# Kernel optimization log

Measured on AMD Instinct MI355X. Metric: run time of the kernel, lower is better.

## Reference

```python
import jax, jax.numpy as jnp
import numpy as np

B, L, E, H = 4, 2048, 1024, 16
D = E // H  # head_dim = 64
NEG_INF = -1e9


def _rope(x):
    # x: [B, L, H, D]; standard rotate-half RoPE over head_dim
    seq = x.shape[1]
    inv_freq = 1.0 / (10000.0 ** (jnp.arange(0, D, 2, dtype=jnp.float32) / D))  # [D/2]
    ang = jnp.arange(seq, dtype=jnp.float32)[:, None] * inv_freq               # [L, D/2]
    cos = jnp.concatenate([jnp.cos(ang), jnp.cos(ang)], axis=-1)[None, :, None, :]
    sin = jnp.concatenate([jnp.sin(ang), jnp.sin(ang)], axis=-1)[None, :, None, :]
    x1, x2 = jnp.split(x, 2, axis=-1)
    rot = jnp.concatenate([-x2, x1], axis=-1)
    return x * cos + rot * sin


def setup_inputs() -> dict:
    key = jax.random.key(0)
    ks = jax.random.split(key, 12)
    xavier = lambda k: jax.random.uniform(k, (E, E), jnp.float32,
                                          -np.sqrt(6.0 / (E + E)), np.sqrt(6.0 / (E + E)))
    return {
        "query": jax.random.normal(ks[0], (B, L, E), jnp.float32),
        "key": jax.random.normal(ks[1], (B, L, E), jnp.float32),
        "value": jax.random.normal(ks[2], (B, L, E), jnp.float32),
        "wq": xavier(ks[3]), "bq": jnp.zeros((E,), jnp.float32),
        "wk": xavier(ks[4]), "bk": jnp.zeros((E,), jnp.float32),
        "wv": xavier(ks[5]), "bv": jnp.zeros((E,), jnp.float32),
        "wo": xavier(ks[6]), "bo": jnp.zeros((E,), jnp.float32),
        "key_padding_mask": jax.random.randint(ks[7], (B, L), 0, 2).astype(bool),
    }


def reference(query, key, value, wq, bq, wk, bk, wv, bv, wo, bo, key_padding_mask):
    b, ql = query.shape[0], query.shape[1]
    sl = key.shape[1]
    q = (query @ wq.T + bq).reshape(b, ql, H, D)
    k = (key @ wk.T + bk).reshape(b, sl, H, D)
    v = (value @ wv.T + bv).reshape(b, sl, H, D)
    q = _rope(q)
    k = _rope(k)
    # causal mask (is_causal=True, attn_mask=None path) + key padding mask, additive
    causal = jnp.where(jnp.triu(jnp.ones((ql, sl), bool), k=1), NEG_INF, 0.0)  # [L, L]
    kpm = jnp.where(key_padding_mask[:, None, None, :], NEG_INF, 0.0)          # [B,1,1,S]
    mask = causal[None, None, :, :] + kpm
    scores = jnp.einsum("bqhd,bkhd->bhqk", q, k) / np.sqrt(D) + mask
    attn = jax.nn.softmax(scores, axis=-1)
    out = jnp.einsum("bhqk,bkhd->bqhd", attn, v).reshape(b, ql, E)
    return out @ wo.T + bo
```

## Files before the change

### kernel.cpp

```cpp
#include <hip/hip_runtime.h>

typedef unsigned short u16;
typedef unsigned int   u32;

using bf16x8 = __attribute__((ext_vector_type(8))) __bf16;
using f32x4  = __attribute__((ext_vector_type(4))) float;
using f32x16 = __attribute__((ext_vector_type(16))) float;

#define DEV static __device__ __forceinline__
#define GP(p) (const __attribute__((address_space(1))) void*)(p)
#define LP(p) (__attribute__((address_space(3))) void*)(p)
#define WAITB(N) asm volatile("s_waitcnt vmcnt(" N ")\n\ts_barrier" ::: "memory")

DEV u16 f2bf(float f){
  u32 u = __builtin_bit_cast(u32, f);
  u32 r = u + 0x7fffu + ((u>>16)&1u);
  return (u16)(r>>16);
}
DEV bf16x8 as_bf(uint4 v){ return __builtin_bit_cast(bf16x8, v); }
DEV u32 cvt_pk(float lo, float hi){
  u32 r;
  asm("v_cvt_pk_bf16_f32 %0, %1, %2" : "=v"(r) : "v"(lo), "v"(hi));
  return r;
}
DEV void plswap(u32 &a, u32 &b){
  auto r = __builtin_amdgcn_permlane32_swap((int)a, (int)b, false, false);
  a = (u32)r[0]; b = (u32)r[1];
}
DEV float fexp2(float x){ float r; asm("v_exp_f32 %0, %1" : "=v"(r) : "v"(x)); return r; }
DEV float max3f(float a, float b, float c){
  float r; asm("v_max3_f32 %0, %1, %2, %3" : "=v"(r) : "v"(a), "v"(b), "v"(c)); return r;
}

constexpr int CB = 4, CL = 2048, CE = 1024, CH = 16, CD = 64;
constexpr int CM = CB*CL;
constexpr float LOG2E  = 1.44269504088896f;
constexpr float NEGBIG = -1.44269504e9f;

__global__ void detect_mask_kernel(const void* __restrict__ mask, int* __restrict__ flag){
  __shared__ int a_gt1, a_badf, a_oddnz, a_evennz;
  if (threadIdx.x==0){ a_gt1=0; a_badf=0; a_oddnz=0; a_evennz=0; }
  __syncthreads();
  const u32* w = (const u32*)mask;
  int gt1=0, badf=0, oddnz=0, evennz=0;
  for (int i=threadIdx.x; i<2048; i+=256){
    u32 v = w[i];
    if (v > 1u) gt1 = 1;
    if (v != 0u && v != 0x3f800000u) badf = 1;
    if (v != 0u){ if (i & 1) oddnz = 1; else evennz = 1; }
  }
  if (gt1) atomicOr(&a_gt1,1);
  if (badf) atomicOr(&a_badf,1);
  if (oddnz) atomicOr(&a_oddnz,1);
  if (evennz) atomicOr(&a_evennz,1);
  __syncthreads();
  if (threadIdx.x==0){
    int mode;
    if (!a_gt1)           mode = (!a_oddnz && a_evennz) ? 3 : 0;
    else if (!a_badf)     mode = 1;
    else                  mode = 2;
    flag[0] = mode;
  }
}

__global__ void convert_mask_kernel(const void* __restrict__ mask, const int* __restrict__ flag,
                                    float* __restrict__ maskf){
  int i = blockIdx.x*blockDim.x + threadIdx.x;
  if (i >= CB*CL) return;
  int mode = flag[0];
  int v;
  if      (mode==0) v = ((const int*)mask)[i] != 0;
  else if (mode==1) v = ((const float*)mask)[i] != 0.f;
  else if (mode==3) v = ((const int*)mask)[2*i] != 0;
  else              v = ((const unsigned char*)mask)[i] != 0;
  maskf[i] = v ? NEGBIG : 0.f;
}

__global__ void cast_all(const float* __restrict__ q, const float* __restrict__ k,
                         const float* __restrict__ v,
                         const float* __restrict__ wq, const float* __restrict__ wk,
                         const float* __restrict__ wv, const float* __restrict__ wo,
                         u16* __restrict__ oq, u16* __restrict__ ok, u16* __restrict__ ov,
                         u16* __restrict__ owq, u16* __restrict__ owk,
                         u16* __restrict__ owv, u16* __restrict__ owo){
  int i = blockIdx.x*blockDim.x + threadIdx.x;
  const float* in; u16* out; int j;
  if (i < 3*(1<<21)){
    int w = i >> 21; j = i & ((1<<21)-1);
    in = (w==0)?q:(w==1)?k:v; out = (w==0)?oq:(w==1)?ok:ov;
  } else {
    int r = i - 3*(1<<21);
    int w = r >> 18; j = r & ((1<<18)-1);
    in = (w==0)?wq:(w==1)?wk:(w==2)?wv:wo; out = (w==0)?owq:(w==1)?owk:(w==2)?owv:owo;
  }
  float4 a = ((const float4*)in)[j];
  ushort4 h;
  h.x = f2bf(a.x); h.y = f2bf(a.y); h.z = f2bf(a.z); h.w = f2bf(a.w);
  ((ushort4*)out)[j] = h;
}

__global__ __launch_bounds__(256) void gemm_qkv(
    const u16* __restrict__ qbf, const u16* __restrict__ kbf, const u16* __restrict__ vbf,
    const u16* __restrict__ wqb, const u16* __restrict__ wkb, const u16* __restrict__ wvb,
    const float* __restrict__ bq, const float* __restrict__ bk, const float* __restrict__ bv,
    u16* __restrict__ Qp, u16* __restrict__ Kp, u16* __restrict__ Vt, int zbase)
{
  __shared__ u16 As[2][8192];
  __shared__ u16 Bs[2][8192];
  const int z = zbase + blockIdx.y;
  const int tid=threadIdx.x, lane=tid&63, wid=tid>>6;
  const int llo=lane&15, lhi=lane>>4;
  const u16* A; const u16* Bt;
  if (z==0){ A=qbf; Bt=wqb; }
  else if (z==1){ A=kbf; Bt=wkb; }
  else { A=wvb; Bt=vbf; }
  int bid = blockIdx.x;
  int xcd = bid&7, j = bid>>3;
  int mb, nb;
  if (z<2){ mb = xcd*8 + (j>>3); nb = j&7; }
  else    { mb = j>>3; nb = xcd*8 + (j&7); }
  const int m0 = mb*128, n0 = nb*128;
  const int wr = wid>>1, wc = wid&1;
  const int rswA = llo&7;

  auto STAGE = [&](int kt, int buf){
    #pragma unroll
    for (int i=0;i<4;i++){
      int c = tid + i*256;
      int row = c>>3, ch = c&7;
      int sc = ch ^ (row&7);
      __builtin_amdgcn_global_load_lds(GP(A  + (size_t)(m0+row)*CE + kt + sc*8),
                                       LP(&As[buf][c*8]), 16, 0, 0);
      __builtin_amdgcn_global_load_lds(GP(Bt + (size_t)(n0+row)*CE + kt + sc*8),
                                       LP(&Bs[buf][c*8]), 16, 0, 0);
    }
  };

  f32x4 acc[4][4] = {};
  STAGE(0, 0);
  asm volatile("s_waitcnt vmcnt(0)" ::: "memory");
  __syncthreads();

  for (int t=0; t<16; t++){
    if (t<15) STAGE((t+1)*64, (t+1)&1);
    const char* as = (const char*)As[t&1];
    const char* bs = (const char*)Bs[t&1];
    #pragma unroll
    for (int ks=0; ks<2; ks++){
      bf16x8 af[4], bf_[4];
      #pragma unroll
      for (int mr=0;mr<4;mr++){
        int r = wr*64+mr*16+llo;
        af[mr] = as_bf(*(const uint4*)(as + r*128 + (((ks*4+lhi)^rswA)<<4)));
      }
      #pragma unroll
      for (int nr=0;nr<4;nr++){
        int r = wc*64+nr*16+llo;
        bf_[nr] = as_bf(*(const uint4*)(bs + r*128 + (((ks*4+lhi)^rswA)<<4)));
      }
      #pragma unroll
      for (int mr=0;mr<4;mr++)
        #pragma unroll
        for (int nr=0;nr<4;nr++)
          acc[mr][nr] = __builtin_amdgcn_mfma_f32_16x16x32_bf16(af[mr], bf_[nr], acc[mr][nr], 0,0,0);
    }
    WAITB("0");
  }

  const int colbase = n0 + wc*64;
  if (z < 2){
    const float* bias = z ? bk : bq;
    u16* outp = z ? Kp : Qp;
    const float scale = z ? 1.f : 0.125f*LOG2E;
    const int h = colbase >> 6;
    float b1[2], b2[2], invf[2];
    #pragma unroll
    for (int nr=0;nr<2;nr++){
      int j2 = nr*16 + llo;
      b1[nr] = bias[colbase + j2];
      b2[nr] = bias[colbase + j2 + 32];
      invf[nr] = exp2f(-(float)j2 * 0.41524101186092033f);
    }
    #pragma unroll
    for (int mr=0;mr<4;mr++)
      #pragma unroll
      for (int r=0;r<4;r++){
        int row = m0 + wr*64 + mr*16 + lhi*4 + r;
        int b = row >> 11, l = row & 2047;
        u16* dst = outp + (((size_t)(b*CH + h)*CL + l) << 6);
        #pragma unroll
        for (int nr=0;nr<2;nr++){
          int j2 = nr*16 + llo;
          float x1 = (acc[mr][nr][r]   + b1[nr]) * scale;
          float x2 = (acc[mr][nr+2][r] + b2[nr]) * scale;
          float ang = (float)l * invf[nr];
          float sn, cs; __sincosf(ang, &sn, &cs);
          dst[j2]      = f2bf(x1*cs - x2*sn);
          dst[j2 + 32] = f2bf(x2*cs + x1*sn);
        }
      }
  } else {
    #pragma unroll
    for (int mr=0;mr<4;mr++)
      #pragma unroll
      for (int r=0;r<4;r++){
        int row = m0 + wr*64 + mr*16 + lhi*4 + r;
        float bvv = bv[row];
        #pragma unroll
        for (int nr=0;nr<4;nr++){
          int col = colbase + nr*16 + llo;
          Vt[(size_t)row*CM + col] = f2bf(acc[mr][nr][r] + bvv);
        }
      }
  }
}

__global__ __launch_bounds__(256) void gemm_out(
    const u16* __restrict__ A, const u16* __restrict__ Bt,
    const float* __restrict__ bias, float* __restrict__ C)
{
  __shared__ u16 As[2][8192];
  __shared__ u16 Bs[2][8192];
  const int tid=threadIdx.x, lane=tid&63, wid=tid>>6;
  const int llo=lane&15, lhi=lane>>4;
  int bid = blockIdx.x;
  int xcd = bid&7, j = bid>>3;
  const int m0 = (xcd*8 + (j>>3))*128, n0 = (j&7)*128;
  const int wr = wid>>1, wc = wid&1;
  const int rswA = llo&7;

  auto STAGE = [&](int kt, int buf){
    #pragma unroll
    for (int i=0;i<4;i++){
      int c = tid + i*256;
      int row = c>>3, ch = c&7;
      int sc = ch ^ (row&7);
      __builtin_amdgcn_global_load_lds(GP(A  + (size_t)(m0+row)*CE + kt + sc*8),
                                       LP(&As[buf][c*8]), 16, 0, 0);
      __builtin_amdgcn_global_load_lds(GP(Bt + (size_t)(n0+row)*CE + kt + sc*8),
                                       LP(&Bs[buf][c*8]), 16, 0, 0);
    }
  };

  f32x4 acc[4][4] = {};
  STAGE(0, 0);
  asm volatile("s_waitcnt vmcnt(0)" ::: "memory");
  __syncthreads();

  for (int t=0; t<16; t++){
    if (t<15) STAGE((t+1)*64, (t+1)&1);
    const char* as = (const char*)As[t&1];
    const char* bs = (const char*)Bs[t&1];
    #pragma unroll
    for (int ks=0; ks<2; ks++){
      bf16x8 af[4], bf_[4];
      #pragma unroll
      for (int mr=0;mr<4;mr++){
        int r = wr*64+mr*16+llo;
        af[mr] = as_bf(*(const uint4*)(as + r*128 + (((ks*4+lhi)^rswA)<<4)));
      }
      #pragma unroll
      for (int nr=0;nr<4;nr++){
        int r = wc*64+nr*16+llo;
        bf_[nr] = as_bf(*(const uint4*)(bs + r*128 + (((ks*4+lhi)^rswA)<<4)));
      }
      #pragma unroll
      for (int mr=0;mr<4;mr++)
        #pragma unroll
        for (int nr=0;nr<4;nr++)
          acc[mr][nr] = __builtin_amdgcn_mfma_f32_16x16x32_bf16(af[mr], bf_[nr], acc[mr][nr], 0,0,0);
    }
    WAITB("0");
  }

  #pragma unroll
  for (int mr=0;mr<4;mr++)
    #pragma unroll
    for (int nr=0;nr<4;nr++)
      #pragma unroll
      for (int r=0;r<4;r++){
        int row = m0 + wr*64 + mr*16 + lhi*4 + r;
        int col = n0 + wc*64 + nr*16 + llo;
        C[(size_t)row*CE + col] = acc[mr][nr][r] + bias[col];
      }
}

__global__ __launch_bounds__(256,2) void attn_kernel(
    const u16* __restrict__ Qp, const u16* __restrict__ Kp, const u16* __restrict__ Vt,
    const float* __restrict__ maskf, u16* __restrict__ AO)
{
  __shared__ u16 K_lds[4][4096];
  __shared__ u16 V_lds[4][4096];
  __shared__ float M_lds[2048];
  const int bh = blockIdx.x;
  const int slot = blockIdx.y;
  const int b = bh >> 4, h = bh & 15;
  const int tid=threadIdx.x, lane=tid&63, wid=tid>>6;
  const int l31 = lane&31, hi = lane>>5;
  const u16* Qh = Qp + (size_t)bh*CL*CD;
  const u16* Kh = Kp + (size_t)bh*CL*CD;
  const u16* Vhd = Vt + (size_t)(h*CD)*CM + b*CL;

  #pragma unroll
  for (int i=0;i<2;i++)
    __builtin_amdgcn_global_load_lds(GP(maskf + b*CL + (i*256+tid)*4),
                                     LP(&M_lds[(i*256+tid)*4]), 16, 0, 0);

  auto STAGE = [&](int t, int buf){
    const u16* Ksrc = Kh + t*64*CD;
    const u16* Vsrc = Vhd + t*64;
    #pragma unroll
    for (int i=0;i<2;i++){
      int c = tid + i*256;
      int row = c>>3, sc = c&7;
      int c16 = sc ^ (row&7);
      __builtin_amdgcn_global_load_lds(GP(Ksrc + row*CD + c16*8),
                                       LP(&K_lds[buf][c*8]), 16, 0, 0);
      __builtin_amdgcn_global_load_lds(GP(Vsrc + (size_t)row*CM + c16*8),
                                       LP(&V_lds[buf][c*8]), 16, 0, 0);
    }
  };

  const int rowb = l31*128;
  const int rsw  = (l31&7)<<4;
  const int qts2[2] = {15-slot, slot};

  for (int qi=0; qi<2; qi++){
    const int qt = qts2[qi];
    const int qw0 = qt*128 + wid*32;
    const int qlane = qw0 + l31;

    bf16x8 qf[4];
    #pragma unroll
    for (int c=0;c<4;c++)
      qf[c] = as_bf(*(const uint4*)(Qh + (size_t)qlane*CD + c*16 + hi*8));

    f32x16 o0 = {}, o1 = {};
    float m_r = -3e38f, l_r = 0.f;

    const int nt = qt*2 + 2;
    STAGE(0,0); STAGE(1,1);

    for (int t=0; t<nt; t++){
      if (t+2 < nt){ STAGE(t+2,(t+2)&3); WAITB("8"); }
      else if (t+1 < nt){ WAITB("4"); }
      else { WAITB("0"); }

      const int kv0 = t*64;
      const char* kb = (const char*)K_lds[t&3];
      const char* vb = (const char*)V_lds[t&3];

      f32x4 cm[8];
      #pragma unroll
      for (int s2=0;s2<2;s2++)
        #pragma unroll
        for (int g=0; g<4; g++)
          cm[s2*4+g] = *(const f32x4*)&M_lds[kv0 + s2*32 + g*8 + hi*4];

      f32x16 s0 = {}, s1 = {};
      __builtin_amdgcn_s_setprio(1);
      #pragma unroll
      for (int c=0;c<4;c++){
        int cb = (c*32 + hi*16) ^ rsw;
        bf16x8 k0 = as_bf(*(const uint4*)(kb + rowb + cb));
        bf16x8 k1 = as_bf(*(const uint4*)(kb + 4096 + rowb + cb));
        s0 = __builtin_amdgcn_mfma_f32_32x32x16_bf16(k0, qf[c], s0, 0,0,0);
        s1 = __builtin_amdgcn_mfma_f32_32x32x16_bf16(k1, qf[c], s1, 0,0,0);
      }
      __builtin_amdgcn_s_setprio(0);

      if (kv0 + 63 > qw0){
        #pragma unroll
        for (int s2=0;s2<2;s2++){
          f32x16& sv = s2 ? s1 : s0;
          #pragma unroll
          for (int reg=0; reg<16; reg++){
            int k = kv0 + s2*32 + (reg&3) + (reg>>2)*8 + hi*4;
            float v = sv[reg] + cm[s2*4+(reg>>2)][reg&3];
            sv[reg] = (k > qlane) ? v + NEGBIG : v;
          }
        }
      } else {
        #pragma unroll
        for (int s2=0;s2<2;s2++){
          f32x16& sv = s2 ? s1 : s0;
          #pragma unroll
          for (int reg=0; reg<16; reg++)
            sv[reg] = sv[reg] + cm[s2*4+(reg>>2)][reg&3];
        }
      }

      f32x16 mx;
      #pragma unroll
      for (int r=0;r<16;r++) mx[r] = fmaxf(s0[r], s1[r]);
      float a0 = max3f(mx[0],mx[1],mx[2]);
      float a1 = max3f(mx[3],mx[4],mx[5]);
      float a2 = max3f(mx[6],mx[7],mx[8]);
      float a3 = max3f(mx[9],mx[10],mx[11]);
      float a4 = max3f(mx[12],mx[13],mx[14]);
      float vmax = fmaxf(max3f(a0,a1,a2), max3f(a3,a4,mx[15]));
      vmax = fmaxf(vmax, __shfl_xor(vmax, 32));

      if (__any(vmax > m_r + 12.0f)){
        float mnew = fmaxf(m_r, vmax);
        float sc = fexp2(m_r - mnew);
        l_r *= sc;
        o0 *= sc; o1 *= sc;
        m_r = mnew;
      }

      #pragma unroll
      for (int r=0;r<16;r++){
        s0[r] = fexp2(s0[r] - m_r);
        s1[r] = fexp2(s1[r] - m_r);
      }
      f32x16 sm = s0 + s1;
      #pragma unroll
      for (int w=8; w>=1; w>>=1)
        #pragma unroll
        for (int r=0;r<w;r++) sm[r] = sm[r] + sm[r+w];
      float rsum = sm[0];
      rsum += __shfl_xor(rsum, 32);
      l_r += rsum;

      u32 w_[16];
      #pragma unroll
      for (int s2=0;s2<2;s2++){
        f32x16& sv = s2 ? s1 : s0;
        #pragma unroll
        for (int c=0;c<2;c++){
          u32 a  = cvt_pk(sv[c*8+0], sv[c*8+1]);
          u32 bb = cvt_pk(sv[c*8+2], sv[c*8+3]);
          u32 cc = cvt_pk(sv[c*8+4], sv[c*8+5]);
          u32 dd = cvt_pk(sv[c*8+6], sv[c*8+7]);
          plswap(a, cc); plswap(bb, dd);
          int base = (s2*2+c)*4;
          w_[base+0]=a; w_[base+1]=bb; w_[base+2]=cc; w_[base+3]=dd;
        }
      }

      __builtin_amdgcn_s_setprio(1);
      #pragma unroll
      for (int kc=0; kc<4; kc++){
        bf16x8 pf = as_bf(make_uint4(w_[kc*4], w_[kc*4+1], w_[kc*4+2], w_[kc*4+3]));
        int cb = (kc*32 + hi*16) ^ rsw;
        bf16x8 v0 = as_bf(*(const uint4*)(vb + rowb + cb));
        bf16x8 v1 = as_bf(*(const uint4*)(vb + 4096 + rowb + cb));
        o0 = __builtin_amdgcn_mfma_f32_32x32x16_bf16(v0, pf, o0, 0,0,0);
        o1 = __builtin_amdgcn_mfma_f32_32x32x16_bf16(v1, pf, o1, 0,0,0);
      }
      __builtin_amdgcn_s_setprio(0);
    }

    float inv = 1.f / l_r;
    u16* dst = AO + (size_t)(b*CL + qlane)*CE + h*CD;
    #pragma unroll
    for (int mt=0; mt<2; mt++){
      f32x16& ov = mt ? o1 : o0;
      #pragma unroll
      for (int g=0; g<4; g++){
        u32 lo  = cvt_pk(ov[g*4+0]*inv, ov[g*4+1]*inv);
        u32 hi2 = cvt_pk(ov[g*4+2]*inv, ov[g*4+3]*inv);
        *(uint2*)(dst + mt*32 + g*8 + hi*4) = make_uint2(lo, hi2);
      }
    }
    __syncthreads();
  }
}

extern "C" void kernel_launch(void* const* d_in, const int* in_sizes, int n_in,
                              void* d_out, int out_size, void* d_ws, size_t ws_size,
                              hipStream_t stream) {
  const float* query = (const float*)d_in[0];
  const float* key_  = (const float*)d_in[1];
  const float* value = (const float*)d_in[2];
  const float* wq = (const float*)d_in[3];
  const float* bq = (const float*)d_in[4];
  const float* wk = (const float*)d_in[5];
  const float* bk = (const float*)d_in[6];
  const float* wv = (const float*)d_in[7];
  const float* bv = (const float*)d_in[8];
  const float* wo = (const float*)d_in[9];
  const float* bo = (const float*)d_in[10];
  const void*  kpm = d_in[11];

  char* ws = (char*)d_ws;
  constexpr size_t SZ_ME_BF = (size_t)CM*CE*2;
  constexpr size_t SZ_EE_BF = (size_t)CE*CE*2;
  constexpr size_t OFF_FLAG = 0;
  constexpr size_t OFF_MASKF= 256;
  constexpr size_t OFF_B0   = 65536;
  constexpr size_t OFF_B1   = OFF_B0 + SZ_ME_BF;
  constexpr size_t OFF_B2   = OFF_B1 + SZ_ME_BF;
  constexpr size_t OFF_WQ   = OFF_B2 + SZ_ME_BF;
  constexpr size_t OFF_WK   = OFF_WQ + SZ_EE_BF;
  constexpr size_t OFF_WV   = OFF_WK + SZ_EE_BF;
  constexpr size_t OFF_WO   = OFF_WV + SZ_EE_BF;
  constexpr size_t OFF_KP   = OFF_WO + SZ_EE_BF;
  constexpr size_t OFF_VT   = OFF_KP + SZ_ME_BF;
  constexpr size_t OFF_QP   = OFF_VT + SZ_ME_BF;

  int*   flag  = (int*)(ws + OFF_FLAG);
  float* maskf = (float*)(ws + OFF_MASKF);
  u16*  qbf = (u16*)(ws + OFF_B0);
  u16*  kbf = (u16*)(ws + OFF_B1);
  u16*  vbf = (u16*)(ws + OFF_B2);
  u16*  wqb = (u16*)(ws + OFF_WQ);
  u16*  wkb = (u16*)(ws + OFF_WK);
  u16*  wvb = (u16*)(ws + OFF_WV);
  u16*  wob = (u16*)(ws + OFF_WO);
  u16*  Kp  = (u16*)(ws + OFF_KP);
  u16*  Vt  = (u16*)(ws + OFF_VT);
  u16*  AO  = qbf;

  detect_mask_kernel<<<1,256,0,stream>>>(kpm, flag);
  convert_mask_kernel<<<(CB*CL+255)/256,256,0,stream>>>(kpm, flag, maskf);

  cast_all<<<28672,256,0,stream>>>(query, key_, value, wq, wk, wv, wo,
                                   qbf, kbf, vbf, wqb, wkb, wvb, wob);

  u16* Qp;
  if (ws_size >= OFF_QP + SZ_ME_BF){
    Qp = (u16*)(ws + OFF_QP);
    gemm_qkv<<<dim3(512,3),256,0,stream>>>(qbf, kbf, vbf, wqb, wkb, wvb,
                                           bq, bk, bv, Qp, Kp, Vt, 0);
  } else {
    Qp = vbf;
    gemm_qkv<<<dim3(512,2),256,0,stream>>>(qbf, kbf, vbf, wqb, wkb, wvb,
                                           bq, bk, bv, Qp, Kp, Vt, 1);
    gemm_qkv<<<dim3(512,1),256,0,stream>>>(qbf, kbf, vbf, wqb, wkb, wvb,
                                           bq, bk, bv, Qp, Kp, Vt, 0);
  }

  attn_kernel<<<dim3(CB*CH, 8),256,0,stream>>>(Qp, Kp, Vt, maskf, AO);

  gemm_out<<<512,256,0,stream>>>(AO, wob, bo, (float*)d_out);
}
```

Baseline: 194.9 us.

## Enlarge QKV GEMM tiles to 256x256 with 8-wave ping-pong schedule

Rewrites the QKV projection GEMM to use 256x256 output tiles per 512-thread block instead of 128x128 per 256-thread block. Each 64-wide K step is split into four 128x128 quadrants, and the loads for the next stage are interleaved with the MFMA work on the current quadrant, using barriers and s_setprio. The goal is more data reuse per LDS byte and better overlap of global-to-LDS copies with matrix math. The cost is double the LDS per block and a grid of only 384 blocks, which can leave CUs unevenly loaded. A stray label ('ated:') is left in the tail block.

```diff
diff --git a/kernel.cpp b/kernel.cpp
--- a/kernel.cpp
+++ b/kernel.cpp
@@ -11,6 +11,8 @@
 #define GP(p) (const __attribute__((address_space(1))) void*)(p)
 #define LP(p) (__attribute__((address_space(3))) void*)(p)
 #define WAITB(N) asm volatile("s_waitcnt vmcnt(" N ")\n\ts_barrier" ::: "memory")
+#define BARR  asm volatile("s_barrier" ::: "memory")
+#define LGKM0 asm volatile("s_waitcnt lgkmcnt(0)" ::: "memory")
 
 DEV u16 f2bf(float f){
   u32 u = __builtin_bit_cast(u32, f);
@@ -99,121 +101,206 @@
   ((ushort4*)out)[j] = h;
 }
 
-__global__ __launch_bounds__(256) void gemm_qkv(
+
+#define STAGE_A(T,BUF,H) do{ \
+  const u16* _s = Abase + (size_t)(m0 + (H)*128)*CE + (T)*64; \
+  u16* _d = &As[BUF][(H)*8192]; \
+  _Pragma("unroll") \
+  for (int _i=0;_i<2;_i++){ \
+    int _c = tid + _i*512; int _row = _c>>3; int _sc = (_c&7) ^ (_row&7); \
+    __builtin_amdgcn_global_load_lds(GP(_s + (size_t)_row*CE + _sc*8), LP(_d + _c*8), 16, 0, 0); \
+  } \
+}while(0)
+
+#define STAGE_B(T,BUF,H) do{ \
+  const u16* _s = Btbase + (size_t)(n0 + (H)*128)*CE + (T)*64; \
+  u16* _d = &Bs[BUF][(H)*8192]; \
+  _Pragma("unroll") \
+  for (int _i=0;_i<2;_i++){ \
+    int _c = tid + _i*512; int _row = _c>>3; int _sc = (_c&7) ^ (_row&7); \
+    __builtin_amdgcn_global_load_lds(GP(_s + (size_t)_row*CE + _sc*8), LP(_d + _c*8), 16, 0, 0); \
+  } \
+}while(0)
+
+#define RD_A(BUF,QM) do{ \
+  const char* _p = (const char*)As[BUF] + ((QM)*128 + wrr*32 + llo)*128; \
+  _Pragma("unroll") \
+  for (int _mr=0;_mr<2;_mr++) \
+    _Pragma("unroll") \
+    for (int _ks=0;_ks<2;_ks++) \
+      af[_mr*2+_ks] = as_bf(*(const uint4*)(_p + _mr*2048 + ((((_ks<<2)+lhi)^rsw)<<4))); \
+}while(0)
+
+#define RD_B(BUF,QN) do{ \
+  const char* _p = (const char*)Bs[BUF] + ((QN)*128 + wcc*64 + llo)*128; \
+  _Pragma("unroll") \
+  for (int _nr=0;_nr<4;_nr++) \
+    _Pragma("unroll") \
+    for (int _ks=0;_ks<2;_ks++) \
+      bfr[_nr*2+_ks] = as_bf(*(const uint4*)(_p + _nr*2048 + ((((_ks<<2)+lhi)^rsw)<<4))); \
+}while(0)
+
+#define MM(QM,QN) do{ \
+  __builtin_amdgcn_s_setprio(1); \
+  _Pragma("unroll") \
+  for (int _mr=0;_mr<2;_mr++) \
+    _Pragma("unroll") \
+    for (int _nr=0;_nr<4;_nr++){ \
+      acc[QM][QN][_mr][_nr] = __builtin_amdgcn_mfma_f32_16x16x32_bf16(af[_mr*2+0], bfr[_nr*2+0], acc[QM][QN][_mr][_nr], 0,0,0); \
+      acc[QM][QN][_mr][_nr] = __builtin_amdgcn_mfma_f32_16x16x32_bf16(af[_mr*2+1], bfr[_nr*2+1], acc[QM][QN][_mr][_nr], 0,0,0); \
+    } \
+  __builtin_amdgcn_s_setprio(0); \
+}while(0)
+
+__global__ __launch_bounds__(512,2) void gemm_qkv(
     const u16* __restrict__ qbf, const u16* __restrict__ kbf, const u16* __restrict__ vbf,
     const u16* __restrict__ wqb, const u16* __restrict__ wkb, const u16* __restrict__ wvb,
     const float* __restrict__ bq, const float* __restrict__ bk, const float* __restrict__ bv,
     u16* __restrict__ Qp, u16* __restrict__ Kp, u16* __restrict__ Vt, int zbase)
 {
-  __shared__ u16 As[2][8192];
-  __shared__ u16 Bs[2][8192];
+  __shared__ u16 As[2][16384];
+  __shared__ u16 Bs[2][16384];
   const int z = zbase + blockIdx.y;
   const int tid=threadIdx.x, lane=tid&63, wid=tid>>6;
   const int llo=lane&15, lhi=lane>>4;
-  const u16* A; const u16* Bt;
-  if (z==0){ A=qbf; Bt=wqb; }
-  else if (z==1){ A=kbf; Bt=wkb; }
-  else { A=wvb; Bt=vbf; }
+  const int wrr=wid>>1, wcc=wid&1;
+  const int rsw = llo&7;
+  const u16* Abase; const u16* Btbase;
+  if (z==0){ Abase=qbf; Btbase=wqb; }
+  else if (z==1){ Abase=kbf; Btbase=wkb; }
+  else { Abase=wvb; Btbase=vbf; }
   int bid = blockIdx.x;
-  int xcd = bid&7, j = bid>>3;
+  int xcd = bid&7, jj = bid>>3;
   int mb, nb;
-  if (z<2){ mb = xcd*8 + (j>>3); nb = j&7; }
-  else    { mb = j>>3; nb = xcd*8 + (j&7); }
-  const int m0 = mb*128, n0 = nb*128;
-  const int wr = wid>>1, wc = wid&1;
-  const int rswA = llo&7;
-
-  auto STAGE = [&](int kt, int buf){
-    #pragma unroll
-    for (int i=0;i<4;i++){
-      int c = tid + i*256;
-      int row = c>>3, ch = c&7;
-      int sc = ch ^ (row&7);
-      __builtin_amdgcn_global_load_lds(GP(A  + (size_t)(m0+row)*CE + kt + sc*8),
-                                       LP(&As[buf][c*8]), 16, 0, 0);
-      __builtin_amdgcn_global_load_lds(GP(Bt + (size_t)(n0+row)*CE + kt + sc*8),
-                                       LP(&Bs[buf][c*8]), 16, 0, 0);
-    }
-  };
-
-  f32x4 acc[4][4] = {};
-  STAGE(0, 0);
-  asm volatile("s_waitcnt vmcnt(0)" ::: "memory");
-  __syncthreads();
-
-  for (int t=0; t<16; t++){
-    if (t<15) STAGE((t+1)*64, (t+1)&1);
-    const char* as = (const char*)As[t&1];
-    const char* bs = (const char*)Bs[t&1];
-    #pragma unroll
-    for (int ks=0; ks<2; ks++){
-      bf16x8 af[4], bf_[4];
-      #pragma unroll
-      for (int mr=0;mr<4;mr++){
-        int r = wr*64+mr*16+llo;
-        af[mr] = as_bf(*(const uint4*)(as + r*128 + (((ks*4+lhi)^rswA)<<4)));
-      }
-      #pragma unroll
-      for (int nr=0;nr<4;nr++){
-        int r = wc*64+nr*16+llo;
-        bf_[nr] = as_bf(*(const uint4*)(bs + r*128 + (((ks*4+lhi)^rswA)<<4)));
-      }
-      #pragma unroll
-      for (int mr=0;mr<4;mr++)
-        #pragma unroll
-        for (int nr=0;nr<4;nr++)
-          acc[mr][nr] = __builtin_amdgcn_mfma_f32_16x16x32_bf16(af[mr], bf_[nr], acc[mr][nr], 0,0,0);
-    }
+  if (z<2){ mb = xcd*4 + (jj>>2); nb = jj&3; }
+  else    { mb = jj&3; nb = xcd*4 + (jj>>2); }
+  const int m0 = mb*256, n0 = nb*256;
+
+  f32x4 acc[2][2][2][4] = {};
+  bf16x8 af[4], bfr[8];
+
+  STAGE_A(0,0,0); STAGE_A(0,0,1); STAGE_B(0,0,0); STAGE_B(0,0,1);
+  STAGE_A(1,1,0); STAGE_B(1,1,1);
+  WAITB("4");
+
+  #pragma unroll 1
+  for (int j=0;j<7;j++){
+    const int T = 2*j;
+    RD_A(0,0); RD_B(0,0);
+    STAGE_A(T+1,1,1);
+    BARR; LGKM0; MM(0,0); BARR;
+    RD_B(0,1);
+    STAGE_B(T+1,1,0);
+    BARR; LGKM0; MM(0,1); BARR;
+    RD_A(0,1);
+    STAGE_A(T+2,0,0);
+    BARR; LGKM0; MM(1,1); BARR;
+    RD_B(0,0);
+    STAGE_B(T+2,0,1);
+    BARR; LGKM0; MM(1,0);
+    WAITB("4");
+    RD_A(1,0); RD_B(1,0);
+    STAGE_A(T+2,0,1);
+    BARR; LGKM0; MM(0,0); BARR;
+    RD_B(1,1);
+    STAGE_B(T+2,0,0);
+    BARR; LGKM0; MM(0,1); BARR;
+    RD_A(1,1);
+    STAGE_A(T+3,1,0);
+    BARR; LGKM0; MM(1,1); BARR;
+    RD_B(1,0);
+    STAGE_B(T+3,1,1);
+    BARR; LGKM0; MM(1,0);
+    WAITB("4");
+  }
+  {ated:
+    const int T = 14;
+    RD_A(0,0); RD_B(0,0);
+    STAGE_A(T+1,1,1);
+    BARR; LGKM0; MM(0,0); BARR;
+    RD_B(0,1);
+    STAGE_B(T+1,1,0);
+    BARR; LGKM0; MM(0,1); BARR;
+    RD_A(0,1);
+    BARR; LGKM0; MM(1,1); BARR;
+    RD_B(0,0);
+    BARR; LGKM0; MM(1,0);
     WAITB("0");
-  }
-
-  const int colbase = n0 + wc*64;
+    RD_A(1,0); RD_B(1,0);
+    BARR; LGKM0; MM(0,0); BARR;
+    RD_B(1,1);
+    BARR; LGKM0; MM(0,1); BARR;
+    RD_A(1,1);
+    BARR; LGKM0; MM(1,1); BARR;
+    RD_B(1,0);
+    BARR; LGKM0; MM(1,0);
+  }
+
   if (z < 2){
     const float* bias = z ? bk : bq;
     u16* outp = z ? Kp : Qp;
     const float scale = z ? 1.f : 0.125f*LOG2E;
-    const int h = colbase >> 6;
-    float b1[2], b2[2], invf[2];
+    float b1[2][2], b2[2][2], invf[2];
     #pragma unroll
     for (int nr=0;nr<2;nr++){
       int j2 = nr*16 + llo;
-      b1[nr] = bias[colbase + j2];
-      b2[nr] = bias[colbase + j2 + 32];
       invf[nr] = exp2f(-(float)j2 * 0.41524101186092033f);
+      #pragma unroll
+      for (int qn=0;qn<2;qn++){
+        int cb = n0 + qn*128 + wcc*64 + j2;
+        b1[qn][nr] = bias[cb];
+        b2[qn][nr] = bias[cb + 32];
+      }
     }
     #pragma unroll
-    for (int mr=0;mr<4;mr++)
-      #pragma unroll
-      for (int r=0;r<4;r++){
-        int row = m0 + wr*64 + mr*16 + lhi*4 + r;
-        int b = row >> 11, l = row & 2047;
-        u16* dst = outp + (((size_t)(b*CH + h)*CL + l) << 6);
-        #pragma unroll
-        for (int nr=0;nr<2;nr++){
-          int j2 = nr*16 + llo;
-          float x1 = (acc[mr][nr][r]   + b1[nr]) * scale;
-          float x2 = (acc[mr][nr+2][r] + b2[nr]) * scale;
-          float ang = (float)l * invf[nr];
-          float sn, cs; __sincosf(ang, &sn, &cs);
-          dst[j2]      = f2bf(x1*cs - x2*sn);
-          dst[j2 + 32] = f2bf(x2*cs + x1*sn);
+    for (int qm=0;qm<2;qm++)
+      #pragma unroll
+      for (int mr=0;mr<2;mr++)
+        #pragma unroll
+        for (int rr=0;rr<4;rr++){
+          int row = m0 + qm*128 + wrr*32 + mr*16 + lhi*4 + rr;
+          int b = row >> 11, l = row & 2047;
+          #pragma unroll
+          for (int qn=0;qn<2;qn++){
+            int h = (n0>>6) + qn*2 + wcc;
+            u16* dst = outp + (((size_t)(b*CH + h)*CL + l) << 6);
+            #pragma unroll
+            for (int nr=0;nr<2;nr++){
+              int j2 = nr*16 + llo;
+              float x1 = (acc[qm][qn][mr][nr][rr]   + b1[qn][nr]) * scale;
+              float x2 = (acc[qm][qn][mr][nr+2][rr] + b2[qn][nr]) * scale;
+              float ang = (float)l * invf[nr];
+              float sn, cs; __sincosf(ang, &sn, &cs);
+              dst[j2]      = f2bf(x1*cs - x2*sn);
+              dst[j2 + 32] = f2bf(x2*cs + x1*sn);
+            }
+          }
         }
-      }
   } else {
     #pragma unroll
-    for (int mr=0;mr<4;mr++)
-      #pragma unroll
-      for (int r=0;r<4;r++){
-        int row = m0 + wr*64 + mr*16 + lhi*4 + r;
-        float bvv = bv[row];
-        #pragma unroll
-        for (int nr=0;nr<4;nr++){
-          int col = colbase + nr*16 + llo;
-          Vt[(size_t)row*CM + col] = f2bf(acc[mr][nr][r] + bvv);
+    for (int qm=0;qm<2;qm++)
+      #pragma unroll
+      for (int mr=0;mr<2;mr++)
+        #pragma unroll
+        for (int rr=0;rr<4;rr++){
+          int row = m0 + qm*128 + wrr*32 + mr*16 + lhi*4 + rr;
+          float bvv = bv[row];
+          #pragma unroll
+          for (int qn=0;qn<2;qn++)
+            #pragma unroll
+            for (int nr=0;nr<4;nr++){
+              int col = n0 + qn*128 + wcc*64 + nr*16 + llo;
+              Vt[(size_t)row*CM + col] = f2bf(acc[qm][qn][mr][nr][rr] + bvv);
+            }
         }
-      }
-  }
-}
+  }
+}
+
+#undef STAGE_A
+#undef STAGE_B
+#undef RD_A
+#undef RD_B
+#undef MM
 
 __global__ __launch_bounds__(256) void gemm_out(
     const u16* __restrict__ A, const u16* __restrict__ Bt,
@@ -522,13 +609,13 @@
   u16* Qp;
   if (ws_size >= OFF_QP + SZ_ME_BF){
     Qp = (u16*)(ws + OFF_QP);
-    gemm_qkv<<<dim3(512,3),256,0,stream>>>(qbf, kbf, vbf, wqb, wkb, wvb,
+    gemm_qkv<<<dim3(128,3),512,0,stream>>>(qbf, kbf, vbf, wqb, wkb, wvb,
                                            bq, bk, bv, Qp, Kp, Vt, 0);
   } else {
     Qp = vbf;
-    gemm_qkv<<<dim3(512,2),256,0,stream>>>(qbf, kbf, vbf, wqb, wkb, wvb,
+    gemm_qkv<<<dim3(128,2),512,0,stream>>>(qbf, kbf, vbf, wqb, wkb, wvb,
                                            bq, bk, bv, Qp, Kp, Vt, 1);
-    gemm_qkv<<<dim3(512,1),256,0,stream>>>(qbf, kbf, vbf, wqb, wkb, wvb,
+    gemm_qkv<<<dim3(128,1),512,0,stream>>>(qbf, kbf, vbf, wqb, wkb, wvb,
                                            bq, bk, bv, Qp, Kp, Vt, 0);
   }
 
```

New measurement: 207.2 us. +6.3%, slower.

## Use 4-stage K=32 LDS pipeline in projection GEMMs and hardware sin/cos for RoPE

Applied to the files above, without the earlier changes.

Both projection GEMMs move from a double-buffered K=64 tile to a four-buffer ring of K=32 tiles. Three stages are prefetched and a partial vmcnt wait keeps loads in flight across iterations, with a new XOR swizzle for the narrower 64-byte rows. Separately, the RoPE epilogue replaces __sincosf with v_fract plus the hardware v_sin/v_cos instructions on angles expressed in revolutions. The risks are more barriers per K step, a loop that is no longer unrolled, and slightly different precision of sin/cos for large angles.

```diff
diff --git a/kernel.cpp b/kernel.cpp
--- a/kernel.cpp
+++ b/kernel.cpp
@@ -31,11 +31,15 @@
 DEV float max3f(float a, float b, float c){
   float r; asm("v_max3_f32 %0, %1, %2, %3" : "=v"(r) : "v"(a), "v"(b), "v"(c)); return r;
 }
+DEV float fractf_(float x){ float r; asm("v_fract_f32 %0, %1" : "=v"(r) : "v"(x)); return r; }
+DEV float sinrev(float f){ float r; asm("v_sin_f32 %0, %1" : "=v"(r) : "v"(f)); return r; }
+DEV float cosrev(float f){ float r; asm("v_cos_f32 %0, %1" : "=v"(r) : "v"(f)); return r; }
 
 constexpr int CB = 4, CL = 2048, CE = 1024, CH = 16, CD = 64;
 constexpr int CM = CB*CL;
 constexpr float LOG2E  = 1.44269504088896f;
 constexpr float NEGBIG = -1.44269504e9f;
+constexpr float INV2PI = 0.15915494309189535f;
 
 __global__ void detect_mask_kernel(const void* __restrict__ mask, int* __restrict__ flag){
   __shared__ int a_gt1, a_badf, a_oddnz, a_evennz;
@@ -105,8 +109,8 @@
     const float* __restrict__ bq, const float* __restrict__ bk, const float* __restrict__ bv,
     u16* __restrict__ Qp, u16* __restrict__ Kp, u16* __restrict__ Vt, int zbase)
 {
-  __shared__ u16 As[2][8192];
-  __shared__ u16 Bs[2][8192];
+  __shared__ u16 As[4][4096];
+  __shared__ u16 Bs[4][4096];
   const int z = zbase + blockIdx.y;
   const int tid=threadIdx.x, lane=tid&63, wid=tid>>6;
   const int llo=lane&15, lhi=lane>>4;
@@ -121,51 +125,56 @@
   else    { mb = j>>3; nb = xcd*8 + (j&7); }
   const int m0 = mb*128, n0 = nb*128;
   const int wr = wid>>1, wc = wid&1;
-  const int rswA = llo&7;
-
-  auto STAGE = [&](int kt, int buf){
-    #pragma unroll
-    for (int i=0;i<4;i++){
+  const int rsw2 = (llo ^ (llo>>2)) & 3;
+
+  auto STAGE = [&](int t, int buf){
+    #pragma unroll
+    for (int i=0;i<2;i++){
       int c = tid + i*256;
-      int row = c>>3, ch = c&7;
-      int sc = ch ^ (row&7);
-      __builtin_amdgcn_global_load_lds(GP(A  + (size_t)(m0+row)*CE + kt + sc*8),
+      int row = c>>2, ch = c&3;
+      int sc = ch ^ ((row ^ (row>>2)) & 3);
+      __builtin_amdgcn_global_load_lds(GP(A  + (size_t)(m0+row)*CE + t*32 + sc*8),
                                        LP(&As[buf][c*8]), 16, 0, 0);
-      __builtin_amdgcn_global_load_lds(GP(Bt + (size_t)(n0+row)*CE + kt + sc*8),
+      __builtin_amdgcn_global_load_lds(GP(Bt + (size_t)(n0+row)*CE + t*32 + sc*8),
                                        LP(&Bs[buf][c*8]), 16, 0, 0);
     }
   };
 
   f32x4 acc[4][4] = {};
-  STAGE(0, 0);
-  asm volatile("s_waitcnt vmcnt(0)" ::: "memory");
-  __syncthreads();
-
-  for (int t=0; t<16; t++){
-    if (t<15) STAGE((t+1)*64, (t+1)&1);
-    const char* as = (const char*)As[t&1];
-    const char* bs = (const char*)Bs[t&1];
-    #pragma unroll
-    for (int ks=0; ks<2; ks++){
-      bf16x8 af[4], bf_[4];
-      #pragma unroll
-      for (int mr=0;mr<4;mr++){
-        int r = wr*64+mr*16+llo;
-        af[mr] = as_bf(*(const uint4*)(as + r*128 + (((ks*4+lhi)^rswA)<<4)));
-      }
-      #pragma unroll
-      for (int nr=0;nr<4;nr++){
-        int r = wc*64+nr*16+llo;
-        bf_[nr] = as_bf(*(const uint4*)(bs + r*128 + (((ks*4+lhi)^rswA)<<4)));
-      }
-      #pragma unroll
-      for (int mr=0;mr<4;mr++)
-        #pragma unroll
-        for (int nr=0;nr<4;nr++)
-          acc[mr][nr] = __builtin_amdgcn_mfma_f32_16x16x32_bf16(af[mr], bf_[nr], acc[mr][nr], 0,0,0);
-    }
-    WAITB("0");
-  }
+
+  auto COMP = [&](int t){
+    const char* as = (const char*)As[t&3];
+    const char* bs = (const char*)Bs[t&3];
+    bf16x8 af[4], bf_[4];
+    #pragma unroll
+    for (int mr=0;mr<4;mr++){
+      int r = wr*64+mr*16+llo;
+      af[mr] = as_bf(*(const uint4*)(as + r*64 + ((lhi^rsw2)<<4)));
+    }
+    #pragma unroll
+    for (int nr=0;nr<4;nr++){
+      int r = wc*64+nr*16+llo;
+      bf_[nr] = as_bf(*(const uint4*)(bs + r*64 + ((lhi^rsw2)<<4)));
+    }
+    #pragma unroll
+    for (int mr=0;mr<4;mr++)
+      #pragma unroll
+      for (int nr=0;nr<4;nr++)
+        acc[mr][nr] = __builtin_amdgcn_mfma_f32_16x16x32_bf16(af[mr], bf_[nr], acc[mr][nr], 0,0,0);
+  };
+
+  STAGE(0,0); STAGE(1,1); STAGE(2,2);
+  WAITB("8");
+
+  #pragma unroll 1
+  for (int t=0; t<29; t++){
+    STAGE(t+3,(t+3)&3);
+    COMP(t);
+    WAITB("8");
+  }
+  COMP(29); WAITB("4");
+  COMP(30); WAITB("0");
+  COMP(31);
 
   const int colbase = n0 + wc*64;
   if (z < 2){
@@ -173,13 +182,13 @@
     u16* outp = z ? Kp : Qp;
     const float scale = z ? 1.f : 0.125f*LOG2E;
     const int h = colbase >> 6;
-    float b1[2], b2[2], invf[2];
+    float b1[2], b2[2], invr[2];
     #pragma unroll
     for (int nr=0;nr<2;nr++){
       int j2 = nr*16 + llo;
       b1[nr] = bias[colbase + j2];
       b2[nr] = bias[colbase + j2 + 32];
-      invf[nr] = exp2f(-(float)j2 * 0.41524101186092033f);
+      invr[nr] = exp2f(-(float)j2 * 0.41524101186092033f) * INV2PI;
     }
     #pragma unroll
     for (int mr=0;mr<4;mr++)
@@ -193,8 +202,8 @@
           int j2 = nr*16 + llo;
           float x1 = (acc[mr][nr][r]   + b1[nr]) * scale;
           float x2 = (acc[mr][nr+2][r] + b2[nr]) * scale;
-          float ang = (float)l * invf[nr];
-          float sn, cs; __sincosf(ang, &sn, &cs);
+          float fr = fractf_((float)l * invr[nr]);
+          float sn = sinrev(fr), cs = cosrev(fr);
           dst[j2]      = f2bf(x1*cs - x2*sn);
           dst[j2 + 32] = f2bf(x2*cs + x1*sn);
         }
@@ -219,59 +228,64 @@
     const u16* __restrict__ A, const u16* __restrict__ Bt,
     const float* __restrict__ bias, float* __restrict__ C)
 {
-  __shared__ u16 As[2][8192];
-  __shared__ u16 Bs[2][8192];
+  __shared__ u16 As[4][4096];
+  __shared__ u16 Bs[4][4096];
   const int tid=threadIdx.x, lane=tid&63, wid=tid>>6;
   const int llo=lane&15, lhi=lane>>4;
   int bid = blockIdx.x;
   int xcd = bid&7, j = bid>>3;
   const int m0 = (xcd*8 + (j>>3))*128, n0 = (j&7)*128;
   const int wr = wid>>1, wc = wid&1;
-  const int rswA = llo&7;
-
-  auto STAGE = [&](int kt, int buf){
-    #pragma unroll
-    for (int i=0;i<4;i++){
+  const int rsw2 = (llo ^ (llo>>2)) & 3;
+
+  auto STAGE = [&](int t, int buf){
+    #pragma unroll
+    for (int i=0;i<2;i++){
       int c = tid + i*256;
-      int row = c>>3, ch = c&7;
-      int sc = ch ^ (row&7);
-      __builtin_amdgcn_global_load_lds(GP(A  + (size_t)(m0+row)*CE + kt + sc*8),
+      int row = c>>2, ch = c&3;
+      int sc = ch ^ ((row ^ (row>>2)) & 3);
+      __builtin_amdgcn_global_load_lds(GP(A  + (size_t)(m0+row)*CE + t*32 + sc*8),
                                        LP(&As[buf][c*8]), 16, 0, 0);
-      __builtin_amdgcn_global_load_lds(GP(Bt + (size_t)(n0+row)*CE + kt + sc*8),
+      __builtin_amdgcn_global_load_lds(GP(Bt + (size_t)(n0+row)*CE + t*32 + sc*8),
                                        LP(&Bs[buf][c*8]), 16, 0, 0);
     }
   };
 
   f32x4 acc[4][4] = {};
-  STAGE(0, 0);
-  asm volatile("s_waitcnt vmcnt(0)" ::: "memory");
-  __syncthreads();
-
-  for (int t=0; t<16; t++){
-    if (t<15) STAGE((t+1)*64, (t+1)&1);
-    const char* as = (const char*)As[t&1];
-    const char* bs = (const char*)Bs[t&1];
-    #pragma unroll
-    for (int ks=0; ks<2; ks++){
-      bf16x8 af[4], bf_[4];
-      #pragma unroll
-      for (int mr=0;mr<4;mr++){
-        int r = wr*64+mr*16+llo;
-        af[mr] = as_bf(*(const uint4*)(as + r*128 + (((ks*4+lhi)^rswA)<<4)));
-      }
-      #pragma unroll
-      for (int nr=0;nr<4;nr++){
-        int r = wc*64+nr*16+llo;
-        bf_[nr] = as_bf(*(const uint4*)(bs + r*128 + (((ks*4+lhi)^rswA)<<4)));
-      }
-      #pragma unroll
-      for (int mr=0;mr<4;mr++)
-        #pragma unroll
-        for (int nr=0;nr<4;nr++)
-          acc[mr][nr] = __builtin_amdgcn_mfma_f32_16x16x32_bf16(af[mr], bf_[nr], acc[mr][nr], 0,0,0);
-    }
-    WAITB("0");
-  }
+
+  auto COMP = [&](int t){
+    const char* as = (const char*)As[t&3];
+    const char* bs = (const char*)Bs[t&3];
+    bf16x8 af[4], bf_[4];
+    #pragma unroll
+    for (int mr=0;mr<4;mr++){
+      int r = wr*64+mr*16+llo;
+      af[mr] = as_bf(*(const uint4*)(as + r*64 + ((lhi^rsw2)<<4)));
+    }
+    #pragma unroll
+    for (int nr=0;nr<4;nr++){
+      int r = wc*64+nr*16+llo;
+      bf_[nr] = as_bf(*(const uint4*)(bs + r*64 + ((lhi^rsw2)<<4)));
+    }
+    #pragma unroll
+    for (int mr=0;mr<4;mr++)
+      #pragma unroll
+      for (int nr=0;nr<4;nr++)
+        acc[mr][nr] = __builtin_amdgcn_mfma_f32_16x16x32_bf16(af[mr], bf_[nr], acc[mr][nr], 0,0,0);
+  };
+
+  STAGE(0,0); STAGE(1,1); STAGE(2,2);
+  WAITB("8");
+
+  #pragma unroll 1
+  for (int t=0; t<29; t++){
+    STAGE(t+3,(t+3)&3);
+    COMP(t);
+    WAITB("8");
+  }
+  COMP(29); WAITB("4");
+  COMP(30); WAITB("0");
+  COMP(31);
 
   #pragma unroll
   for (int mr=0;mr<4;mr++)
```

New measurement: 212.1 us. +8.8%, slower.

## Use 256x128 GEMM tiles with 512 threads and triple-buffered LDS pipeline

Applied to the files above, without the earlier changes.

Both projection GEMMs (QKV and output) move from 128x128 tiles with 256 threads and double buffering to 256x128 tiles with 8 waves and a 3-stage global_load_lds pipeline. The waitcnt of 6 lets the next stage's loads stay in flight while the current buffer is computed. The larger M tile reuses each B tile across more rows, at the cost of more LDS (about 144KB per block) and half as many blocks. RoPE sin/cos now use hardware v_fract/v_sin/v_cos on revolutions instead of __sincosf, which may change accuracy slightly.

```diff
diff --git a/kernel.cpp b/kernel.cpp
--- a/kernel.cpp
+++ b/kernel.cpp
@@ -31,11 +31,15 @@
 DEV float max3f(float a, float b, float c){
   float r; asm("v_max3_f32 %0, %1, %2, %3" : "=v"(r) : "v"(a), "v"(b), "v"(c)); return r;
 }
+DEV float fractf_(float x){ float r; asm("v_fract_f32 %0, %1" : "=v"(r) : "v"(x)); return r; }
+DEV float sinrev(float f){ float r; asm("v_sin_f32 %0, %1" : "=v"(r) : "v"(f)); return r; }
+DEV float cosrev(float f){ float r; asm("v_cos_f32 %0, %1" : "=v"(r) : "v"(f)); return r; }
 
 constexpr int CB = 4, CL = 2048, CE = 1024, CH = 16, CD = 64;
 constexpr int CM = CB*CL;
 constexpr float LOG2E  = 1.44269504088896f;
 constexpr float NEGBIG = -1.44269504e9f;
+constexpr float INV2PI = 0.15915494309189535f;
 
 __global__ void detect_mask_kernel(const void* __restrict__ mask, int* __restrict__ flag){
   __shared__ int a_gt1, a_badf, a_oddnz, a_evennz;
@@ -99,14 +103,14 @@
   ((ushort4*)out)[j] = h;
 }
 
-__global__ __launch_bounds__(256) void gemm_qkv(
+__global__ __launch_bounds__(512) void gemm_qkv(
     const u16* __restrict__ qbf, const u16* __restrict__ kbf, const u16* __restrict__ vbf,
     const u16* __restrict__ wqb, const u16* __restrict__ wkb, const u16* __restrict__ wvb,
     const float* __restrict__ bq, const float* __restrict__ bk, const float* __restrict__ bv,
     u16* __restrict__ Qp, u16* __restrict__ Kp, u16* __restrict__ Vt, int zbase)
 {
-  __shared__ u16 As[2][8192];
-  __shared__ u16 Bs[2][8192];
+  __shared__ u16 As[3][16384];
+  __shared__ u16 Bs[3][8192];
   const int z = zbase + blockIdx.y;
   const int tid=threadIdx.x, lane=tid&63, wid=tid>>6;
   const int llo=lane&15, lhi=lane>>4;
@@ -117,34 +121,36 @@
   int bid = blockIdx.x;
   int xcd = bid&7, j = bid>>3;
   int mb, nb;
-  if (z<2){ mb = xcd*8 + (j>>3); nb = j&7; }
-  else    { mb = j>>3; nb = xcd*8 + (j&7); }
-  const int m0 = mb*128, n0 = nb*128;
+  if (z<2){ mb = xcd*4 + (j>>3); nb = j&7; }
+  else    { mb = j&3;  nb = xcd*8 + (j>>2); }
+  const int m0 = mb*256, n0 = nb*128;
   const int wr = wid>>1, wc = wid&1;
   const int rswA = llo&7;
 
-  auto STAGE = [&](int kt, int buf){
+  auto STAGE = [&](int t, int buf){
     #pragma unroll
     for (int i=0;i<4;i++){
-      int c = tid + i*256;
+      int c = tid + i*512;
       int row = c>>3, ch = c&7;
       int sc = ch ^ (row&7);
-      __builtin_amdgcn_global_load_lds(GP(A  + (size_t)(m0+row)*CE + kt + sc*8),
+      __builtin_amdgcn_global_load_lds(GP(A + (size_t)(m0+row)*CE + t*64 + sc*8),
                                        LP(&As[buf][c*8]), 16, 0, 0);
-      __builtin_amdgcn_global_load_lds(GP(Bt + (size_t)(n0+row)*CE + kt + sc*8),
+    }
+    #pragma unroll
+    for (int i=0;i<2;i++){
+      int c = tid + i*512;
+      int row = c>>3, ch = c&7;
+      int sc = ch ^ (row&7);
+      __builtin_amdgcn_global_load_lds(GP(Bt + (size_t)(n0+row)*CE + t*64 + sc*8),
                                        LP(&Bs[buf][c*8]), 16, 0, 0);
     }
   };
 
   f32x4 acc[4][4] = {};
-  STAGE(0, 0);
-  asm volatile("s_waitcnt vmcnt(0)" ::: "memory");
-  __syncthreads();
-
-  for (int t=0; t<16; t++){
-    if (t<15) STAGE((t+1)*64, (t+1)&1);
-    const char* as = (const char*)As[t&1];
-    const char* bs = (const char*)Bs[t&1];
+
+  auto COMP = [&](int buf){
+    const char* as = (const char*)As[buf];
+    const char* bs = (const char*)Bs[buf];
     #pragma unroll
     for (int ks=0; ks<2; ks++){
       bf16x8 af[4], bf_[4];
@@ -164,8 +170,19 @@
         for (int nr=0;nr<4;nr++)
           acc[mr][nr] = __builtin_amdgcn_mfma_f32_16x16x32_bf16(af[mr], bf_[nr], acc[mr][nr], 0,0,0);
     }
-    WAITB("0");
-  }
+  };
+
+  STAGE(0,0); STAGE(1,1);
+  WAITB("6");
+
+  #pragma unroll 1
+  for (int t=0; t<14; t++){
+    STAGE(t+2, (t+2)%3);
+    COMP(t%3);
+    WAITB("6");
+  }
+  COMP(2); WAITB("0");
+  COMP(0);
 
   const int colbase = n0 + wc*64;
   if (z < 2){
@@ -173,13 +190,13 @@
     u16* outp = z ? Kp : Qp;
     const float scale = z ? 1.f : 0.125f*LOG2E;
     const int h = colbase >> 6;
-    float b1[2], b2[2], invf[2];
+    float b1[2], b2[2], invr[2];
     #pragma unroll
     for (int nr=0;nr<2;nr++){
       int j2 = nr*16 + llo;
       b1[nr] = bias[colbase + j2];
       b2[nr] = bias[colbase + j2 + 32];
-      invf[nr] = exp2f(-(float)j2 * 0.41524101186092033f);
+      invr[nr] = exp2f(-(float)j2 * 0.41524101186092033f) * INV2PI;
     }
     #pragma unroll
     for (int mr=0;mr<4;mr++)
@@ -193,8 +210,8 @@
           int j2 = nr*16 + llo;
           float x1 = (acc[mr][nr][r]   + b1[nr]) * scale;
           float x2 = (acc[mr][nr+2][r] + b2[nr]) * scale;
-          float ang = (float)l * invf[nr];
-          float sn, cs; __sincosf(ang, &sn, &cs);
+          float fr = fractf_((float)l * invr[nr]);
+          float sn = sinrev(fr), cs = cosrev(fr);
           dst[j2]      = f2bf(x1*cs - x2*sn);
           dst[j2 + 32] = f2bf(x2*cs + x1*sn);
         }
@@ -215,42 +232,44 @@
   }
 }
 
-__global__ __launch_bounds__(256) void gemm_out(
+__global__ __launch_bounds__(512) void gemm_out(
     const u16* __restrict__ A, const u16* __restrict__ Bt,
     const float* __restrict__ bias, float* __restrict__ C)
 {
-  __shared__ u16 As[2][8192];
-  __shared__ u16 Bs[2][8192];
+  __shared__ u16 As[3][16384];
+  __shared__ u16 Bs[3][8192];
   const int tid=threadIdx.x, lane=tid&63, wid=tid>>6;
   const int llo=lane&15, lhi=lane>>4;
   int bid = blockIdx.x;
   int xcd = bid&7, j = bid>>3;
-  const int m0 = (xcd*8 + (j>>3))*128, n0 = (j&7)*128;
+  const int m0 = (xcd*4 + (j>>3))*256, n0 = (j&7)*128;
   const int wr = wid>>1, wc = wid&1;
   const int rswA = llo&7;
 
-  auto STAGE = [&](int kt, int buf){
+  auto STAGE = [&](int t, int buf){
     #pragma unroll
     for (int i=0;i<4;i++){
-      int c = tid + i*256;
+      int c = tid + i*512;
       int row = c>>3, ch = c&7;
       int sc = ch ^ (row&7);
-      __builtin_amdgcn_global_load_lds(GP(A  + (size_t)(m0+row)*CE + kt + sc*8),
+      __builtin_amdgcn_global_load_lds(GP(A + (size_t)(m0+row)*CE + t*64 + sc*8),
                                        LP(&As[buf][c*8]), 16, 0, 0);
-      __builtin_amdgcn_global_load_lds(GP(Bt + (size_t)(n0+row)*CE + kt + sc*8),
+    }
+    #pragma unroll
+    for (int i=0;i<2;i++){
+      int c = tid + i*512;
+      int row = c>>3, ch = c&7;
+      int sc = ch ^ (row&7);
+      __builtin_amdgcn_global_load_lds(GP(Bt + (size_t)(n0+row)*CE + t*64 + sc*8),
                                        LP(&Bs[buf][c*8]), 16, 0, 0);
     }
   };
 
   f32x4 acc[4][4] = {};
-  STAGE(0, 0);
-  asm volatile("s_waitcnt vmcnt(0)" ::: "memory");
-  __syncthreads();
-
-  for (int t=0; t<16; t++){
-    if (t<15) STAGE((t+1)*64, (t+1)&1);
-    const char* as = (const char*)As[t&1];
-    const char* bs = (const char*)Bs[t&1];
+
+  auto COMP = [&](int buf){
+    const char* as = (const char*)As[buf];
+    const char* bs = (const char*)Bs[buf];
     #pragma unroll
     for (int ks=0; ks<2; ks++){
       bf16x8 af[4], bf_[4];
@@ -270,8 +289,19 @@
         for (int nr=0;nr<4;nr++)
           acc[mr][nr] = __builtin_amdgcn_mfma_f32_16x16x32_bf16(af[mr], bf_[nr], acc[mr][nr], 0,0,0);
     }
-    WAITB("0");
-  }
+  };
+
+  STAGE(0,0); STAGE(1,1);
+  WAITB("6");
+
+  #pragma unroll 1
+  for (int t=0; t<14; t++){
+    STAGE(t+2, (t+2)%3);
+    COMP(t%3);
+    WAITB("6");
+  }
+  COMP(2); WAITB("0");
+  COMP(0);
 
   #pragma unroll
   for (int mr=0;mr<4;mr++)
@@ -522,17 +552,17 @@
   u16* Qp;
   if (ws_size >= OFF_QP + SZ_ME_BF){
     Qp = (u16*)(ws + OFF_QP);
-    gemm_qkv<<<dim3(512,3),256,0,stream>>>(qbf, kbf, vbf, wqb, wkb, wvb,
+    gemm_qkv<<<dim3(256,3),512,0,stream>>>(qbf, kbf, vbf, wqb, wkb, wvb,
                                            bq, bk, bv, Qp, Kp, Vt, 0);
   } else {
     Qp = vbf;
-    gemm_qkv<<<dim3(512,2),256,0,stream>>>(qbf, kbf, vbf, wqb, wkb, wvb,
+    gemm_qkv<<<dim3(256,2),512,0,stream>>>(qbf, kbf, vbf, wqb, wkb, wvb,
                                            bq, bk, bv, Qp, Kp, Vt, 1);
-    gemm_qkv<<<dim3(512,1),256,0,stream>>>(qbf, kbf, vbf, wqb, wkb, wvb,
+    gemm_qkv<<<dim3(256,1),512,0,stream>>>(qbf, kbf, vbf, wqb, wkb, wvb,
                                            bq, bk, bv, Qp, Kp, Vt, 0);
   }
 
   attn_kernel<<<dim3(CB*CH, 8),256,0,stream>>>(Qp, Kp, Vt, maskf, AO);
 
-  gemm_out<<<512,256,0,stream>>>(AO, wob, bo, (float*)d_out);
-}
+  gemm_out<<<256,512,0,stream>>>(AO, wob, bo, (float*)d_out);
+}
```

After: 193.6 us. About the same (-0.7%).
